# Performance work log

Measured on AMD Instinct MI355X. Metric: run time of the kernel, lower is better.

The kernel has to match this reference:

```python
import jax, jax.numpy as jnp
import numpy as np
from jax import lax

B, T, H, E, V, S = 32, 512, 1024, 300, 32000, 50
NL2 = 4  # 2 layers * 2 directions of encoder hidden


def setup_inputs() -> dict:
    key = jax.random.key(0)
    ks = jax.random.split(key, 20)
    w = 0.05  # small init scale to keep tanh/softmax well-conditioned
    return {
        "enc_out": jax.random.normal(ks[0], (B, T, H), jnp.float32),
        "enc_h": jax.random.normal(ks[1], (NL2, B, H // 2), jnp.float32),
        "enc_c": jax.random.normal(ks[2], (NL2, B, H // 2), jnp.float32),
        "embedding": jax.random.normal(ks[3], (V, E), jnp.float32),
        "attn_W": jax.random.normal(ks[4], (H, 2 * H), jnp.float32) * w,
        "attn_b": jnp.zeros((H,), jnp.float32),
        "v": jax.random.normal(ks[5], (H,), jnp.float32) * w,
        "Wih0": jax.random.normal(ks[6], (4 * H, E + H), jnp.float32) * w,
        "Whh0": jax.random.normal(ks[7], (4 * H, H), jnp.float32) * w,
        "bih0": jnp.zeros((4 * H,), jnp.float32),
        "bhh0": jnp.zeros((4 * H,), jnp.float32),
        "Wih1": jax.random.normal(ks[8], (4 * H, H), jnp.float32) * w,
        "Whh1": jax.random.normal(ks[9], (4 * H, H), jnp.float32) * w,
        "bih1": jnp.zeros((4 * H,), jnp.float32),
        "bhh1": jnp.zeros((4 * H,), jnp.float32),
        "genW": jax.random.normal(ks[10], (V, H), jnp.float32) * w,
        "genb": jnp.zeros((V,), jnp.float32),
        "question": jax.random.randint(ks[11], (B, S), 0, V, jnp.int64),
    }


def _lstm_cell(x, h, c, Wih, Whh, bih, bhh):
    # torch gate order: i, f, g, o
    g = x @ Wih.T + bih + h @ Whh.T + bhh
    i, f, gg, o = jnp.split(g, 4, axis=-1)
    c2 = jax.nn.sigmoid(f) * c + jax.nn.sigmoid(i) * jnp.tanh(gg)
    h2 = jax.nn.sigmoid(o) * jnp.tanh(c2)
    return h2, c2


def reference(enc_out, enc_h, enc_c, embedding, attn_W, attn_b, v,
              Wih0, Whh0, bih0, bhh0, Wih1, Whh1, bih1, bhh1,
              genW, genb, question):
    # merge bidirectional encoder halves: (2L,B,H/2) -> (L,B,H)
    h0 = jnp.concatenate([enc_h[0::2], enc_h[1::2]], axis=2)
    c0 = jnp.concatenate([enc_c[0::2], enc_c[1::2]], axis=2)

    def step(carry, tok):
        h, c = carry  # each (L, B, H)
        emb = embedding[tok]  # (B, E); dropout is identity (eval mode)
        hid = h[-1]  # (B, H), last-layer hidden drives attention
        Hrep = jnp.broadcast_to(hid[:, None, :], enc_out.shape)  # (B,T,H)
        energy = jnp.tanh(jnp.concatenate([Hrep, enc_out], axis=-1) @ attn_W.T + attn_b)
        scores = jnp.einsum('bth,h->bt', energy, v)
        aw = jax.nn.softmax(scores, axis=1)  # (B, T)
        ctx = jnp.einsum('bt,bth->bh', aw, enc_out)  # (B, H)
        x = jnp.concatenate([emb, ctx], axis=-1)  # (B, E+H)
        h0n, c0n = _lstm_cell(x, h[0], c[0], Wih0, Whh0, bih0, bhh0)
        h1n, c1n = _lstm_cell(h0n, h[1], c[1], Wih1, Whh1, bih1, bhh1)
        out = jax.nn.log_softmax(h1n @ genW.T + genb, axis=-1)  # (B, V)
        return (jnp.stack([h0n, h1n]), jnp.stack([c0n, c1n])), out

    _, outs = lax.scan(step, (h0, c0), question.T)  # outs: (S, B, V)
    return jnp.transpose(outs, (1, 0, 2))  # (B, S, V)
```

## Files before the change

kernel.cpp:

```cpp
#include <hip/hip_runtime.h>
#include <hip/hip_bf16.h>
#include <math.h>

#define DEVI static __device__ __forceinline__

namespace {
constexpr int B = 32, T = 512, H = 1024, E = 300, V = 32000, S = 50;
constexpr int KX = E + H;
constexpr int K0 = 2368;
constexpr int K1 = 2048;
constexpr int MG = V + H;
}

typedef __bf16 bf16x8 __attribute__((ext_vector_type(8)));
typedef float f32x4 __attribute__((ext_vector_type(4)));

DEVI float bf2f(unsigned short u) { union { unsigned int i; float f; } v; v.i = (unsigned int)u << 16; return v.f; }
DEVI unsigned short f2bf(float f) {
  union { float f; unsigned int i; } v; v.f = f;
  unsigned int x = v.i;
  return (unsigned short)((x + 0x7fffu + ((x >> 16) & 1u)) >> 16);
}
#if __has_builtin(__builtin_amdgcn_rcpf)
DEVI float frcp(float x) { return __builtin_amdgcn_rcpf(x); }
#else
DEVI float frcp(float x) { return 1.0f / x; }
#endif
DEVI float sigm(float x) { return frcp(1.0f + __expf(-x)); }
DEVI float tanh_(float x) { return 1.0f - 2.0f * frcp(__expf(2.0f * x) + 1.0f); }

__global__ __launch_bounds__(256) void k_cast_gen(const float* __restrict__ genW,
    const float* __restrict__ attn_W, unsigned short* __restrict__ Wbig) {
  size_t i4 = ((size_t)blockIdx.x * 256 + threadIdx.x) * 4;
  if (i4 >= (size_t)MG * H) return;
  int row = (int)(i4 >> 10), k = (int)(i4 & 1023);
  const float* src = row < V ? &genW[((size_t)row << 10) + k]
                             : &attn_W[(size_t)(row - V) * (2 * H) + k];
  float4 v = *(const float4*)src;
  ushort4 o; o.x = f2bf(v.x); o.y = f2bf(v.y); o.z = f2bf(v.z); o.w = f2bf(v.w);
  *(ushort4*)&Wbig[i4] = o;
}

__global__ __launch_bounds__(256) void k_cast_l0(const float* __restrict__ Wih,
    const float* __restrict__ Whh, unsigned short* __restrict__ Wc) {
  int m = blockIdx.x;
  int g = m & 3, n = m >> 2, srow = g * H + n;
  for (int i = threadIdx.x; i < K0 / 4; i += 256) {
    int k = i * 4;
    float4 v;
    if (k < KX) v = *(const float4*)&Wih[(size_t)srow * KX + k];
    else if (k < KX + H) v = *(const float4*)&Whh[(size_t)srow * H + (k - KX)];
    else v = make_float4(0.f, 0.f, 0.f, 0.f);
    ushort4 o; o.x = f2bf(v.x); o.y = f2bf(v.y); o.z = f2bf(v.z); o.w = f2bf(v.w);
    *(ushort4*)&Wc[(size_t)m * K0 + k] = o;
  }
}

__global__ __launch_bounds__(256) void k_cast_l1(const float* __restrict__ Wih,
    const float* __restrict__ Whh, unsigned short* __restrict__ Wc) {
  int m = blockIdx.x;
  int g = m & 3, n = m >> 2, srow = g * H + n;
  for (int i = threadIdx.x; i < K1 / 4; i += 256) {
    int k = i * 4;
    float4 v = (k < H) ? *(const float4*)&Wih[(size_t)srow * H + k]
                       : *(const float4*)&Whh[(size_t)srow * H + (k - H)];
    ushort4 o; o.x = f2bf(v.x); o.y = f2bf(v.y); o.z = f2bf(v.z); o.w = f2bf(v.w);
    *(ushort4*)&Wc[(size_t)m * K1 + k] = o;
  }
}

__global__ __launch_bounds__(256) void k_cast_attnr(const float* __restrict__ attn_W,
                                                    unsigned short* __restrict__ Wr) {
  size_t i4 = ((size_t)blockIdx.x * 256 + threadIdx.x) * 4;
  if (i4 >= (size_t)H * H) return;
  int n = (int)(i4 >> 10), k = (int)(i4 & 1023);
  float4 v = *(const float4*)&attn_W[(size_t)n * (2 * H) + H + k];
  ushort4 o; o.x = f2bf(v.x); o.y = f2bf(v.y); o.z = f2bf(v.z); o.w = f2bf(v.w);
  *(ushort4*)&Wr[i4] = o;
}

__global__ void k_bias(const float* bih0, const float* bhh0,
                       const float* bih1, const float* bhh1,
                       float* bc0, float* bc1) {
  int idx = blockIdx.x * 256 + threadIdx.x;
  if (idx < 4096) { int g = idx & 3, n = idx >> 2; bc0[idx] = bih0[g * H + n] + bhh0[g * H + n]; }
  else if (idx < 8192) { int m = idx - 4096; int g = m & 3, n = m >> 2; bc1[m] = bih1[g * H + n] + bhh1[g * H + n]; }
}

__global__ __launch_bounds__(256) void k_cast_enc(const float* __restrict__ src,
                                                  unsigned short* __restrict__ dst) {
  size_t i4 = ((size_t)blockIdx.x * 256 + threadIdx.x) * 4;
  if (i4 >= (size_t)B * T * H) return;
  float4 v = *(const float4*)&src[i4];
  ushort4 o; o.x = f2bf(v.x); o.y = f2bf(v.y); o.z = f2bf(v.z); o.w = f2bf(v.w);
  *(ushort4*)&dst[i4] = o;
}

__global__ __launch_bounds__(256) void k_init(const float* __restrict__ enc_h,
    const float* __restrict__ enc_c, float* __restrict__ cbuf,
    unsigned short* __restrict__ xc0_0, unsigned short* __restrict__ xc0_1,
    unsigned short* __restrict__ xc1_0, unsigned short* __restrict__ hgen) {
  int idx = blockIdx.x * 256 + threadIdx.x;
  if (idx < 2 * B * H) {
    int l = idx >> 15, r = idx & 32767, b = r >> 10, hh = r & 1023;
    int half = hh >> 9, hr = hh & 511;
    int src = (2 * l + half) * B * (H / 2) + b * (H / 2) + hr;
    cbuf[idx] = enc_c[src];
    unsigned short hb = f2bf(enc_h[src]);
    if (l == 0) xc0_0[(size_t)b * K0 + KX + hh] = hb;
    else { xc1_0[(size_t)b * K1 + H + hh] = hb; hgen[(size_t)b * H + hh] = hb; }
  } else if (idx < 2 * B * H + 2 * B * 20) {
    int j = idx - 2 * B * H;
    int p = j / (B * 20), rr = j % (B * 20), b = rr / 20, kk = rr % 20;
    (p ? xc0_1 : xc0_0)[(size_t)b * K0 + KX + H + kk] = 0;
  }
}

__global__ __launch_bounds__(256) void k_encproj_mfma(const unsigned short* __restrict__ Wr,
    const unsigned short* __restrict__ Xb, const float* __restrict__ attn_b,
    unsigned short* __restrict__ encp) {
  int wv = threadIdx.x >> 6, lane = threadIdx.x & 63;
  int n0w = blockIdx.x * 64 + wv * 16;
  int m0 = blockIdx.y * 64;
  const unsigned short* Wp = Wr + (size_t)(n0w + (lane & 15)) * H + (lane >> 4) * 8;
  const unsigned short* Xp = Xb + (size_t)(m0 + (lane & 15)) * H + (lane >> 4) * 8;
  f32x4 acc[4] = {{0.f,0.f,0.f,0.f},{0.f,0.f,0.f,0.f},{0.f,0.f,0.f,0.f},{0.f,0.f,0.f,0.f}};
#pragma unroll 2
  for (int k0 = 0; k0 < H; k0 += 32) {
    bf16x8 a = *(const bf16x8*)(Wp + k0);
#pragma unroll
    for (int g = 0; g < 4; g++) {
      bf16x8 b = *(const bf16x8*)(Xp + (size_t)g * 16 * H + k0);
      acc[g] = __builtin_amdgcn_mfma_f32_16x16x32_bf16(a, b, acc[g], 0, 0, 0);
    }
  }
  int nb = n0w + (lane >> 4) * 4;
  f32x4 bi = *(const f32x4*)&attn_b[nb];
#pragma unroll
  for (int g = 0; g < 4; g++) {
    int m = m0 + g * 16 + (lane & 15);
    f32x4 o = acc[g] + bi;
    ushort4 ob; ob.x = f2bf(o[0]); ob.y = f2bf(o[1]); ob.z = f2bf(o[2]); ob.w = f2bf(o[3]);
    *(ushort4*)&encp[(size_t)m * H + nb] = ob;
  }
}

template <int K>
DEVI void gemm_tile(const unsigned short* __restrict__ W, const unsigned short* __restrict__ X,
                    int m0w, int lane, f32x4& acc0, f32x4& acc1) {
  const unsigned short* Wp = W + (size_t)(m0w + (lane & 15)) * K + (lane >> 4) * 8;
  const unsigned short* Xp = X + (size_t)(lane & 15) * K + (lane >> 4) * 8;
#pragma unroll 4
  for (int k0 = 0; k0 < K; k0 += 32) {
    bf16x8 a  = *(const bf16x8*)(Wp + k0);
    bf16x8 b0 = *(const bf16x8*)(Xp + k0);
    bf16x8 b1 = *(const bf16x8*)(Xp + 16 * K + k0);
    acc0 = __builtin_amdgcn_mfma_f32_16x16x32_bf16(a, b0, acc0, 0, 0, 0);
    acc1 = __builtin_amdgcn_mfma_f32_16x16x32_bf16(a, b1, acc1, 0, 0, 0);
  }
}

template <int K>
__global__ __launch_bounds__(256) void k_gemm_out(const unsigned short* __restrict__ W,
    const unsigned short* __restrict__ X, const float* __restrict__ bias, int M0,
    float* __restrict__ out0, int ld0, float* __restrict__ out1, int ld1,
    float* __restrict__ part) {
  __shared__ float esum[4][32];
  int wv = threadIdx.x >> 6, lane = threadIdx.x & 63;
  int m0w = blockIdx.x * 64 + wv * 16;
  f32x4 acc0 = {0.f, 0.f, 0.f, 0.f}, acc1 = acc0;
  gemm_tile<K>(W, X, m0w, lane, acc0, acc1);
  int r0 = m0w + (lane >> 4) * 4;
  int b = lane & 15;
  float s0 = 0.f, s1 = 0.f;
  if (r0 < M0) {
    f32x4 bi = *(const f32x4*)&bias[r0];
    f32x4 o0 = acc0 + bi, o1 = acc1 + bi;
    *(f32x4*)&out0[(size_t)b * ld0 + r0] = o0;
    *(f32x4*)&out0[(size_t)(b + 16) * ld0 + r0] = o1;
    s0 = __expf(o0[0]) + __expf(o0[1]) + __expf(o0[2]) + __expf(o0[3]);
    s1 = __expf(o1[0]) + __expf(o1[1]) + __expf(o1[2]) + __expf(o1[3]);
  } else {
    int r = r0 - M0;
    *(f32x4*)&out1[(size_t)b * ld1 + r] = acc0;
    *(f32x4*)&out1[(size_t)(b + 16) * ld1 + r] = acc1;
  }
  if (part != nullptr && blockIdx.x < V / 64) {
    s0 += __shfl_xor(s0, 16, 64); s0 += __shfl_xor(s0, 32, 64);
    s1 += __shfl_xor(s1, 16, 64); s1 += __shfl_xor(s1, 32, 64);
    if (lane < 16) { esum[wv][lane] = s0; esum[wv][lane + 16] = s1; }
    __syncthreads();
    if (threadIdx.x < 32)
      part[blockIdx.x * 32 + threadIdx.x] =
          esum[0][threadIdx.x] + esum[1][threadIdx.x] + esum[2][threadIdx.x] + esum[3][threadIdx.x];
  }
}

template <int K>
__global__ __launch_bounds__(256) void k_gemm_lstm(const unsigned short* __restrict__ W,
    const unsigned short* __restrict__ X, const float* __restrict__ bcomb,
    float* __restrict__ c,
    unsigned short* __restrict__ hA, int ldA_, int offA,
    unsigned short* __restrict__ hB, int ldB_, int offB) {
  __shared__ f32x4 red[4][64][2];
  int wv = threadIdx.x >> 6, lane = threadIdx.x & 63;
  int m0w = blockIdx.x * 16;
  const unsigned short* Wp = W + (size_t)(m0w + (lane & 15)) * K + (lane >> 4) * 8;
  const unsigned short* Xp = X + (size_t)(lane & 15) * K + (lane >> 4) * 8;
  f32x4 acc0 = {0.f, 0.f, 0.f, 0.f}, acc1 = acc0;
#pragma unroll 2
  for (int k0 = wv * 32; k0 < K; k0 += 128) {
    bf16x8 a  = *(const bf16x8*)(Wp + k0);
    bf16x8 b0 = *(const bf16x8*)(Xp + k0);
    bf16x8 b1 = *(const bf16x8*)(Xp + 16 * K + k0);
    acc0 = __builtin_amdgcn_mfma_f32_16x16x32_bf16(a, b0, acc0, 0, 0, 0);
    acc1 = __builtin_amdgcn_mfma_f32_16x16x32_bf16(a, b1, acc1, 0, 0, 0);
  }
  red[wv][lane][0] = acc0;
  red[wv][lane][1] = acc1;
  __syncthreads();
  if (wv == 0) {
    acc0 = red[0][lane][0] + red[1][lane][0] + red[2][lane][0] + red[3][lane][0];
    acc1 = red[0][lane][1] + red[1][lane][1] + red[2][lane][1] + red[3][lane][1];
    int r0 = m0w + (lane >> 4) * 4;
    int n = r0 >> 2;
    f32x4 bi = *(const f32x4*)&bcomb[r0];
#pragma unroll
    for (int f = 0; f < 2; f++) {
      f32x4 g = f ? acc1 : acc0;
      int b = (lane & 15) + f * 16;
      float gi = g[0] + bi[0], gf = g[1] + bi[1];
      float gg = g[2] + bi[2], go = g[3] + bi[3];
      float cp = c[(size_t)b * H + n];
      float c2 = sigm(gf) * cp + sigm(gi) * tanh_(gg);
      c[(size_t)b * H + n] = c2;
      unsigned short hb = f2bf(sigm(go) * tanh_(c2));
      hA[(size_t)b * ldA_ + offA + n] = hb;
      hB[(size_t)b * ldB_ + offB + n] = hb;
    }
  }
}

__global__ __launch_bounds__(256) void k_scores(const unsigned short* __restrict__ encp,
    const float* __restrict__ hidproj, const float* __restrict__ vvec,
    float* __restrict__ scores) {
  int wid = blockIdx.x * 4 + (threadIdx.x >> 6);
  int lane = threadIdx.x & 63;
  int b = wid >> 9;
  const unsigned short* ep = encp + (size_t)wid * H;
  const float* hp = hidproj + (size_t)b * H;
  float acc = 0.f;
#pragma unroll
  for (int i = 0; i < 2; i++) {
    int base = i * 512 + lane * 8;
    uint4 u = *(const uint4*)&ep[base];
    float4 h0 = *(const float4*)&hp[base];
    float4 h1 = *(const float4*)&hp[base + 4];
    float4 v0 = *(const float4*)&vvec[base];
    float4 v1 = *(const float4*)&vvec[base + 4];
    acc += v0.x * tanh_(bf2f((unsigned short)(u.x & 0xffff)) + h0.x);
    acc += v0.y * tanh_(bf2f((unsigned short)(u.x >> 16)) + h0.y);
    acc += v0.z * tanh_(bf2f((unsigned short)(u.y & 0xffff)) + h0.z);
    acc += v0.w * tanh_(bf2f((unsigned short)(u.y >> 16)) + h0.w);
    acc += v1.x * tanh_(bf2f((unsigned short)(u.z & 0xffff)) + h1.x);
    acc += v1.y * tanh_(bf2f((unsigned short)(u.z >> 16)) + h1.y);
    acc += v1.z * tanh_(bf2f((unsigned short)(u.w & 0xffff)) + h1.z);
    acc += v1.w * tanh_(bf2f((unsigned short)(u.w >> 16)) + h1.w);
  }
#pragma unroll
  for (int off = 32; off; off >>= 1) acc += __shfl_xor(acc, off, 64);
  if (lane == 0) scores[wid] = acc;
}

__global__ __launch_bounds__(256) void k_ctx(const float* __restrict__ scores,
    const unsigned short* __restrict__ enc_bf, const float* __restrict__ embedding,
    const int* __restrict__ question, int s, unsigned short* __restrict__ xc) {
  int b = blockIdx.x, y = blockIdx.y, tid = threadIdx.x;
  if (y == 16) {
    int tok = question[b * S + s];
    for (int e = tid; e < E; e += 256)
      xc[(size_t)b * K0 + e] = f2bf(embedding[(size_t)tok * E + e]);
    return;
  }
  __shared__ float aw[T];
  __shared__ float red[256];
  float s0 = scores[b * T + tid], s1 = scores[b * T + 256 + tid];
  float m = fmaxf(s0, s1);
  red[tid] = m; __syncthreads();
  for (int st = 128; st; st >>= 1) { if (tid < st) red[tid] = fmaxf(red[tid], red[tid + st]); __syncthreads(); }
  m = red[0]; __syncthreads();
  float e0 = __expf(s0 - m), e1 = __expf(s1 - m);
  aw[tid] = e0; aw[tid + 256] = e1;
  red[tid] = e0 + e1; __syncthreads();
  for (int st = 128; st; st >>= 1) { if (tid < st) red[tid] += red[tid + st]; __syncthreads(); }
  float inv = frcp(red[0]);
  __syncthreads();
  int wv = tid >> 6, l = tid & 63;
  int q = l & 15, tp = l >> 4;
  const unsigned short* eb = enc_bf + (size_t)b * T * H + y * 64 + q * 4;
  float a0 = 0.f, a1 = 0.f, a2 = 0.f, a3 = 0.f;
  for (int it = 0; it < 32; it++) {
    int t = it * 16 + wv * 4 + tp;
    uint2 u = *(const uint2*)&eb[(size_t)t * H];
    float w = aw[t];
    a0 += w * bf2f((unsigned short)(u.x & 0xffff));
    a1 += w * bf2f((unsigned short)(u.x >> 16));
    a2 += w * bf2f((unsigned short)(u.y & 0xffff));
    a3 += w * bf2f((unsigned short)(u.y >> 16));
  }
  a0 += __shfl_xor(a0, 16, 64); a0 += __shfl_xor(a0, 32, 64);
  a1 += __shfl_xor(a1, 16, 64); a1 += __shfl_xor(a1, 32, 64);
  a2 += __shfl_xor(a2, 16, 64); a2 += __shfl_xor(a2, 32, 64);
  a3 += __shfl_xor(a3, 16, 64); a3 += __shfl_xor(a3, 32, 64);
  __syncthreads();
  if (tp == 0) {
    red[wv * 64 + q * 4 + 0] = a0; red[wv * 64 + q * 4 + 1] = a1;
    red[wv * 64 + q * 4 + 2] = a2; red[wv * 64 + q * 4 + 3] = a3;
  }
  __syncthreads();
  if (tid < 64) {
    float val = (red[tid] + red[64 + tid] + red[128 + tid] + red[192 + tid]) * inv;
    xc[(size_t)b * K0 + E + y * 64 + tid] = f2bf(val);
  }
}

__global__ __launch_bounds__(256) void k_lsB(const float* __restrict__ logits,
    const float* __restrict__ part, float* __restrict__ out, int s) {
  int b = blockIdx.x, ch = blockIdx.y, tid = threadIdx.x;
  __shared__ float red[256];
  float ssum = 0.f;
  for (int i = tid; i < V / 64; i += 256) ssum += part[i * 32 + b];
  red[tid] = ssum; __syncthreads();
  for (int st = 128; st; st >>= 1) { if (tid < st) red[tid] += red[tid + st]; __syncthreads(); }
  float lse = __logf(red[0]);
  const float* L = logits + (size_t)b * V + ch * 4000;
  float* O = out + ((size_t)b * S + s) * V + ch * 4000;
  for (int i = tid; i < 1000; i += 256) {
    float4 v = ((const float4*)L)[i];
    ((float4*)O)[i] = make_float4(v.x - lse, v.y - lse, v.z - lse, v.w - lse);
  }
}

extern "C" void kernel_launch(void* const* d_in, const int* in_sizes, int n_in,
                              void* d_out, int out_size, void* d_ws, size_t ws_size,
                              hipStream_t stream) {
  const float* enc_out   = (const float*)d_in[0];
  const float* enc_h     = (const float*)d_in[1];
  const float* enc_c     = (const float*)d_in[2];
  const float* embedding = (const float*)d_in[3];
  const float* attn_W    = (const float*)d_in[4];
  const float* attn_b    = (const float*)d_in[5];
  const float* vvec      = (const float*)d_in[6];
  const float* Wih0      = (const float*)d_in[7];
  const float* Whh0      = (const float*)d_in[8];
  const float* bih0      = (const float*)d_in[9];
  const float* bhh0      = (const float*)d_in[10];
  const float* Wih1      = (const float*)d_in[11];
  const float* Whh1      = (const float*)d_in[12];
  const float* bih1      = (const float*)d_in[13];
  const float* bhh1      = (const float*)d_in[14];
  const float* genW      = (const float*)d_in[15];
  const float* genb      = (const float*)d_in[16];
  const int*   question  = (const int*)d_in[17];
  float* out = (float*)d_out;

  char* w = (char*)d_ws;
  auto alloc = [&](size_t bytes) { char* r = w; w += (bytes + 255) & ~(size_t)255; return r; };
  unsigned short* Wbig  = (unsigned short*)alloc((size_t)MG * H * 2);
  unsigned short* Wc0   = (unsigned short*)alloc((size_t)4096 * K0 * 2);
  unsigned short* Wc1   = (unsigned short*)alloc((size_t)4096 * K1 * 2);
  unsigned short* encb  = (unsigned short*)alloc((size_t)B * T * H * 2);
  unsigned short* encp  = (unsigned short*)alloc((size_t)B * T * H * 2);
  unsigned short* Wr    = (unsigned short*)alloc((size_t)H * H * 2);
  float* bcomb0 = (float*)alloc(4096 * 4);
  float* bcomb1 = (float*)alloc(4096 * 4);
  float* cbuf   = (float*)alloc((size_t)2 * B * H * 4);
  unsigned short* xc0[2] = {(unsigned short*)alloc((size_t)B * K0 * 2),
                            (unsigned short*)alloc((size_t)B * K0 * 2)};
  unsigned short* xc1[2] = {(unsigned short*)alloc((size_t)B * K1 * 2),
                            (unsigned short*)alloc((size_t)B * K1 * 2)};
  unsigned short* hgen  = (unsigned short*)alloc((size_t)B * H * 2);
  float* hidproj = (float*)alloc((size_t)B * H * 4);
  float* scores  = (float*)alloc((size_t)B * T * 4);
  float* logits  = (float*)alloc((size_t)B * V * 4);
  float* part    = (float*)alloc((size_t)(V / 64) * 32 * 4);

  k_cast_gen<<<(int)(((size_t)MG * H / 4 + 255) / 256), 256, 0, stream>>>(genW, attn_W, Wbig);
  k_cast_l0<<<4096, 256, 0, stream>>>(Wih0, Whh0, Wc0);
  k_cast_l1<<<4096, 256, 0, stream>>>(Wih1, Whh1, Wc1);
  k_cast_attnr<<<H * H / 4 / 256, 256, 0, stream>>>(attn_W, Wr);
  k_bias<<<32, 256, 0, stream>>>(bih0, bhh0, bih1, bhh1, bcomb0, bcomb1);
  k_cast_enc<<<(B * T * H / 4) / 256, 256, 0, stream>>>(enc_out, encb);
  k_init<<<(2 * B * H + 2 * B * 20 + 255) / 256, 256, 0, stream>>>(
      enc_h, enc_c, cbuf, xc0[0], xc0[1], xc1[0], hgen);
  k_encproj_mfma<<<dim3(H / 64, B * T / 64), 256, 0, stream>>>(Wr, encb, attn_b, encp);
  k_gemm_out<1024><<<H / 64, 256, 0, stream>>>(
      Wbig + (size_t)V * H, hgen, nullptr, 0, nullptr, 0, hidproj, H, nullptr);

  for (int s = 0; s < S; s++) {
    int par = s & 1;
    k_scores<<<B * T / 4, 256, 0, stream>>>(encp, hidproj, vvec, scores);
    k_ctx<<<dim3(B, 17), 256, 0, stream>>>(scores, encb, embedding, question, s, xc0[par]);
    k_gemm_lstm<K0><<<4096 / 16, 256, 0, stream>>>(
        Wc0, xc0[par], bcomb0, cbuf,
        xc0[par ^ 1], K0, KX,
        xc1[par], K1, 0);
    k_gemm_lstm<K1><<<4096 / 16, 256, 0, stream>>>(
        Wc1, xc1[par], bcomb1, cbuf + B * H,
        xc1[par ^ 1], K1, H,
        hgen, H, 0);
    k_gemm_out<1024><<<MG / 64, 256, 0, stream>>>(
        Wbig, hgen, genb, V, logits, V, hidproj, H, part);
    k_lsB<<<dim3(B, 8), 256, 0, stream>>>(logits, part, out, s);
  }
}
```

Baseline: 4.096 ms.

## Fuse scores, previous-step log-softmax write and embedding gather into one launch

Combines the attention-score kernel, the embedding gather, and the log-softmax output write of the previous step into a single heterogeneous kernel, dispatching on block index. The log-softmax for step s is deferred into step s+1's first kernel, and a final standalone launch handles the last step. This removes one kernel launch per step and lets the memory-bound output write overlap with the score computation. It relies on logits/part not being overwritten before the fused kernel reads them; since the output GEMM runs later in the same step, that ordering holds.

```diff
diff --git a/kernel.cpp b/kernel.cpp
--- a/kernel.cpp
+++ b/kernel.cpp
@@ -241,47 +241,68 @@
   }
 }
 
-__global__ __launch_bounds__(256) void k_scores(const unsigned short* __restrict__ encp,
+__global__ __launch_bounds__(256) void k_p1(const unsigned short* __restrict__ encp,
     const float* __restrict__ hidproj, const float* __restrict__ vvec,
-    float* __restrict__ scores) {
-  int wid = blockIdx.x * 4 + (threadIdx.x >> 6);
-  int lane = threadIdx.x & 63;
-  int b = wid >> 9;
-  const unsigned short* ep = encp + (size_t)wid * H;
-  const float* hp = hidproj + (size_t)b * H;
-  float acc = 0.f;
+    float* __restrict__ scores,
+    const float* __restrict__ logits, const float* __restrict__ part,
+    float* __restrict__ out,
+    const float* __restrict__ embedding, const int* __restrict__ question,
+    unsigned short* __restrict__ xc, int s) {
+  int bx = blockIdx.x, tid = threadIdx.x;
+  if (bx < 4096) {
+    int wid = bx * 4 + (tid >> 6);
+    int lane = tid & 63;
+    int b = wid >> 9;
+    const unsigned short* ep = encp + (size_t)wid * H;
+    const float* hp = hidproj + (size_t)b * H;
+    float acc = 0.f;
 #pragma unroll
-  for (int i = 0; i < 2; i++) {
-    int base = i * 512 + lane * 8;
-    uint4 u = *(const uint4*)&ep[base];
-    float4 h0 = *(const float4*)&hp[base];
-    float4 h1 = *(const float4*)&hp[base + 4];
-    float4 v0 = *(const float4*)&vvec[base];
-    float4 v1 = *(const float4*)&vvec[base + 4];
-    acc += v0.x * tanh_(bf2f((unsigned short)(u.x & 0xffff)) + h0.x);
-    acc += v0.y * tanh_(bf2f((unsigned short)(u.x >> 16)) + h0.y);
-    acc += v0.z * tanh_(bf2f((unsigned short)(u.y & 0xffff)) + h0.z);
-    acc += v0.w * tanh_(bf2f((unsigned short)(u.y >> 16)) + h0.w);
-    acc += v1.x * tanh_(bf2f((unsigned short)(u.z & 0xffff)) + h1.x);
-    acc += v1.y * tanh_(bf2f((unsigned short)(u.z >> 16)) + h1.y);
-    acc += v1.z * tanh_(bf2f((unsigned short)(u.w & 0xffff)) + h1.z);
-    acc += v1.w * tanh_(bf2f((unsigned short)(u.w >> 16)) + h1.w);
-  }
+    for (int i = 0; i < 2; i++) {
+      int base = i * 512 + lane * 8;
+      uint4 u = *(const uint4*)&ep[base];
+      float4 h0 = *(const float4*)&hp[base];
+      float4 h1 = *(const float4*)&hp[base + 4];
+      float4 v0 = *(const float4*)&vvec[base];
+      float4 v1 = *(const float4*)&vvec[base + 4];
+      acc += v0.x * tanh_(bf2f((unsigned short)(u.x & 0xffff)) + h0.x);
+      acc += v0.y * tanh_(bf2f((unsigned short)(u.x >> 16)) + h0.y);
+      acc += v0.z * tanh_(bf2f((unsigned short)(u.y & 0xffff)) + h0.z);
+      acc += v0.w * tanh_(bf2f((unsigned short)(u.y >> 16)) + h0.w);
+      acc += v1.x * tanh_(bf2f((unsigned short)(u.z & 0xffff)) + h1.x);
+      acc += v1.y * tanh_(bf2f((unsigned short)(u.z >> 16)) + h1.y);
+      acc += v1.z * tanh_(bf2f((unsigned short)(u.w & 0xffff)) + h1.z);
+      acc += v1.w * tanh_(bf2f((unsigned short)(u.w >> 16)) + h1.w);
+    }
 #pragma unroll
-  for (int off = 32; off; off >>= 1) acc += __shfl_xor(acc, off, 64);
-  if (lane == 0) scores[wid] = acc;
-}
-
-__global__ __launch_bounds__(256) void k_ctx(const float* __restrict__ scores,
-    const unsigned short* __restrict__ enc_bf, const float* __restrict__ embedding,
-    const int* __restrict__ question, int s, unsigned short* __restrict__ xc) {
-  int b = blockIdx.x, y = blockIdx.y, tid = threadIdx.x;
-  if (y == 16) {
+    for (int off = 32; off; off >>= 1) acc += __shfl_xor(acc, off, 64);
+    if (lane == 0) scores[wid] = acc;
+  } else if (bx < 4352) {
+    if (s == 0) return;
+    __shared__ float red[256];
+    int idx = bx - 4096;
+    int b = idx >> 3, ch = idx & 7;
+    float ssum = 0.f;
+    for (int i = tid; i < V / 64; i += 256) ssum += part[i * 32 + b];
+    red[tid] = ssum; __syncthreads();
+    for (int st = 128; st; st >>= 1) { if (tid < st) red[tid] += red[tid + st]; __syncthreads(); }
+    float lse = __logf(red[0]);
+    const float* L = logits + (size_t)b * V + ch * 4000;
+    float* O = out + ((size_t)b * S + (s - 1)) * V + ch * 4000;
+    for (int i = tid; i < 1000; i += 256) {
+      float4 v = ((const float4*)L)[i];
+      ((float4*)O)[i] = make_float4(v.x - lse, v.y - lse, v.z - lse, v.w - lse);
+    }
+  } else {
+    int b = bx - 4352;
     int tok = question[b * S + s];
     for (int e = tid; e < E; e += 256)
       xc[(size_t)b * K0 + e] = f2bf(embedding[(size_t)tok * E + e]);
-    return;
-  }
+  }
+}
+
+__global__ __launch_bounds__(256) void k_ctx(const float* __restrict__ scores,
+    const unsigned short* __restrict__ enc_bf, unsigned short* __restrict__ xc) {
+  int b = blockIdx.x, y = blockIdx.y, tid = threadIdx.x;
   __shared__ float aw[T];
   __shared__ float red[256];
   float s0 = scores[b * T + tid], s1 = scores[b * T + 256 + tid];
@@ -399,8 +420,9 @@
 
   for (int s = 0; s < S; s++) {
     int par = s & 1;
-    k_scores<<<B * T / 4, 256, 0, stream>>>(encp, hidproj, vvec, scores);
-    k_ctx<<<dim3(B, 17), 256, 0, stream>>>(scores, encb, embedding, question, s, xc0[par]);
+    k_p1<<<4384, 256, 0, stream>>>(encp, hidproj, vvec, scores,
+                                   logits, part, out, embedding, question, xc0[par], s);
+    k_ctx<<<dim3(B, 16), 256, 0, stream>>>(scores, encb, xc0[par]);
     k_gemm_lstm<K0><<<4096 / 16, 256, 0, stream>>>(
         Wc0, xc0[par], bcomb0, cbuf,
         xc0[par ^ 1], K0, KX,
@@ -411,6 +433,6 @@
         hgen, H, 0);
     k_gemm_out<1024><<<MG / 64, 256, 0, stream>>>(
         Wbig, hgen, genb, V, logits, V, hidproj, H, part);
-    k_lsB<<<dim3(B, 8), 256, 0, stream>>>(logits, part, out, s);
-  }
-}
+  }
+  k_lsB<<<dim3(B, 8), 256, 0, stream>>>(logits, part, out, S - 1);
+}
```

After: 3.957 ms. -3.4%, faster.
